# Kernel tuning notes

Measured on AMD Instinct MI355X. Metric: run time of the kernel, lower is better.

## Reference

```python
import jax, jax.numpy as jnp
import numpy as np

B, T_ENC, T_DEC = 32, 300, 500
N_MEL, ENC_DIM, ATT_RNN, DEC_RNN, PRE = 80, 512, 1024, 1024, 256
ATT_DIM, LOC_F, LOC_K = 128, 32, 31
PAD = (LOC_K - 1) // 2
P_PRENET = 0.1


def _w(k, shape, fan_in):
    return jax.random.normal(k, shape, jnp.float32) / np.float32(np.sqrt(fan_in))


def setup_inputs() -> dict:
    key = jax.random.key(0)
    ks = jax.random.split(key, 20)
    lens = jax.random.randint(ks[2], (B,), T_ENC // 2, T_ENC + 1).at[0].set(T_ENC)
    return {
        "memory": jax.random.normal(ks[0], (B, T_ENC, ENC_DIM), jnp.float32),
        "decoder_inputs": jax.random.normal(ks[1], (B, N_MEL, T_DEC), jnp.float32),
        "memory_lengths": lens,
        "pre_W1": _w(ks[3], (PRE, N_MEL), N_MEL),
        "pre_W2": _w(ks[4], (PRE, PRE), PRE),
        "att_Wih": _w(ks[5], (4 * ATT_RNN, PRE + ENC_DIM), PRE + ENC_DIM),
        "att_Whh": _w(ks[6], (4 * ATT_RNN, ATT_RNN), ATT_RNN),
        "att_bih": jnp.zeros((4 * ATT_RNN,), jnp.float32),
        "att_bhh": jnp.zeros((4 * ATT_RNN,), jnp.float32),
        "q_W": _w(ks[7], (ATT_DIM, ATT_RNN), ATT_RNN),
        "m_W": _w(ks[8], (ATT_DIM, ENC_DIM), ENC_DIM),
        "v_w": _w(ks[9], (ATT_DIM,), ATT_DIM),
        "loc_conv_W": _w(ks[10], (LOC_F, 2, LOC_K), 2 * LOC_K),
        "loc_dense_W": _w(ks[11], (ATT_DIM, LOC_F), LOC_F),
        "dec_Wih": _w(ks[12], (4 * DEC_RNN, ATT_RNN + ENC_DIM), ATT_RNN + ENC_DIM),
        "dec_Whh": _w(ks[13], (4 * DEC_RNN, DEC_RNN), DEC_RNN),
        "dec_bih": jnp.zeros((4 * DEC_RNN,), jnp.float32),
        "dec_bhh": jnp.zeros((4 * DEC_RNN,), jnp.float32),
        "proj_W": _w(ks[14], (N_MEL, DEC_RNN + ENC_DIM), DEC_RNN + ENC_DIM),
        "proj_b": jnp.zeros((N_MEL,), jnp.float32),
        "gate_W": _w(ks[15], (DEC_RNN + ENC_DIM,), DEC_RNN + ENC_DIM),
        "gate_b": jnp.zeros((), jnp.float32),
    }


def _lstm(x, h, c, Wih, Whh, bih, bhh):
    # PyTorch LSTMCell gate order: i, f, g, o
    g = x @ Wih.T + bih + h @ Whh.T + bhh
    i, f, gg, o = jnp.split(g, 4, axis=-1)
    c = jax.nn.sigmoid(f) * c + jax.nn.sigmoid(i) * jnp.tanh(gg)
    h = jax.nn.sigmoid(o) * jnp.tanh(c)
    return h, c


def _prenet(x, W1, W2):
    # Original uses F.dropout(..., 0.1, training=True) always; deterministic masks here.
    k1, k2 = jax.random.split(jax.random.key(1))
    x = jax.nn.relu(x @ W1.T)
    x = x * jax.random.bernoulli(k1, 1.0 - P_PRENET, x.shape) / (1.0 - P_PRENET)
    x = jax.nn.relu(x @ W2.T)
    x = x * jax.random.bernoulli(k2, 1.0 - P_PRENET, x.shape) / (1.0 - P_PRENET)
    return x


def _forward(memory, decoder_inputs, memory_lengths, pre_W1, pre_W2, att_Wih, att_Whh,
             att_bih, att_bhh, q_W, m_W, v_w, loc_conv_W, loc_dense_W, dec_Wih, dec_Whh,
             dec_bih, dec_bhh, proj_W, proj_b, gate_W, gate_b):
    x = jnp.transpose(decoder_inputs, (2, 0, 1))          # [T_dec, B, n_mel]
    go = jnp.zeros((1,) + x.shape[1:], x.dtype)
    x = jnp.concatenate([go, x], axis=0)                  # [T_dec+1, B, n_mel]
    dec_ins = _prenet(x, pre_W1, pre_W2)[:-1]             # [T_dec, B, PRE]

    processed_memory = memory @ m_W.T                     # [B, T_enc, ATT_DIM]
    valid = jnp.arange(T_ENC)[None, :] < memory_lengths[:, None]  # [B, T_enc]
    Bn = memory.shape[0]
    zf = lambda d: jnp.zeros((Bn, d), memory.dtype)
    carry0 = (zf(ATT_RNN), zf(ATT_RNN), zf(DEC_RNN), zf(DEC_RNN),
              zf(T_ENC), zf(T_ENC), zf(ENC_DIM))

    def step(carry, x_t):
        ah, ac, dh, dc, aw, awc, ctx = carry
        ah, ac = _lstm(jnp.concatenate([x_t, ctx], 1), ah, ac,
                       att_Wih, att_Whh, att_bih, att_bhh)
        awcat = jnp.stack([aw, awc], axis=1)              # [B, 2, T_enc]
        loc = jax.lax.conv_general_dilated(awcat, loc_conv_W, (1,), [(PAD, PAD)],
                                           dimension_numbers=('NCH', 'OIH', 'NCH'))
        loc = jnp.transpose(loc, (0, 2, 1)) @ loc_dense_W.T   # [B, T_enc, ATT_DIM]
        pq = (ah @ q_W.T)[:, None, :]                     # [B, 1, ATT_DIM]
        e = jnp.tanh(pq + loc + processed_memory) @ v_w   # [B, T_enc]
        e = jnp.where(valid, e, -jnp.inf)
        aw = jax.nn.softmax(e, axis=1)
        ctx = jnp.einsum('bt,btd->bd', aw, memory)        # [B, ENC_DIM]
        awc = awc + aw
        dh, dc = _lstm(jnp.concatenate([ah, ctx], 1), dh, dc,
                       dec_Wih, dec_Whh, dec_bih, dec_bhh)
        dhac = jnp.concatenate([dh, ctx], 1)
        mel = dhac @ proj_W.T + proj_b                    # [B, n_mel]
        gate = dhac @ gate_W + gate_b                     # [B]
        return (ah, ac, dh, dc, aw, awc, ctx), (mel, gate, aw)

    _, (mels, gates, aligns) = jax.lax.scan(jax.checkpoint(step), carry0, dec_ins)
    mel_outputs = jnp.transpose(mels, (1, 2, 0))          # [B, n_mel, T_dec]
    gate_outputs = gates.T                                # [B, T_dec]
    alignments = jnp.transpose(aligns, (1, 0, 2))         # [B, T_dec, T_enc]
    return mel_outputs, gate_outputs, alignments


def reference(memory, decoder_inputs, memory_lengths, pre_W1, pre_W2, att_Wih, att_Whh,
              att_bih, att_bhh, q_W, m_W, v_w, loc_conv_W, loc_dense_W, dec_Wih, dec_Whh,
              dec_bih, dec_bhh, proj_W, proj_b, gate_W, gate_b):
    return _forward(memory, decoder_inputs, memory_lengths, pre_W1, pre_W2, att_Wih,
                    att_Whh, att_bih, att_bhh, q_W, m_W, v_w, loc_conv_W, loc_dense_W,
                    dec_Wih, dec_Whh, dec_bih, dec_bhh, proj_W, proj_b, gate_W, gate_b)
```

## Files before the change

kernel.cpp:

```cpp
#include <hip/hip_runtime.h>

#define NB 32
#define TENC 300
#define TDEC 500
#define NMEL 80
#define ENCD 512
#define PRE 256
#define ADIM 128
#define RD 4
#define WSPLIT 2944

#define OFF_DECINS 0ull
#define OFF_WHI    2048000ull
#define OFF_AHR    4096000ull
#define OFF_DHR    (OFF_AHR + 131072ull)
#define OFF_CXR    (OFF_DHR + 131072ull)
#define RINGS_N    327680ull
#define OFF_WLO    (OFF_AHR + RINGS_N)
#define OFF_PM     8192000ull
#define OFF_STATE  (OFF_PM + 1228800ull)
#define OFF_AC     (OFF_STATE + 0ull)
#define OFF_DC     (OFF_STATE + 32768ull)
#define OFF_AW     (OFF_STATE + 65536ull)
#define OFF_AWC    (OFF_STATE + 75136ull)
#define OFF_E      (OFF_STATE + 84736ull)
#define OFF_SLOTS  (OFF_STATE + 94336ull)
#define STATE_N    98440ull
#define OFF_QWT    (OFF_STATE + STATE_N)
#define OFF_PROJWT (OFF_QWT + 131072ull)
#define OFF_MWT    (OFF_PROJWT + 122880ull)
#define OFF_W1T    (OFF_MWT + 65536ull)
#define OFF_W2T    (OFF_W1T + 20480ull)

__device__ __forceinline__ unsigned short f2bf(float f){
  unsigned u = __float_as_uint(f);
  unsigned r = (u + 0x7FFFu + ((u >> 16) & 1u)) >> 16;
  return (unsigned short)r;
}
__device__ __forceinline__ float bf2f(unsigned short h){
  return __uint_as_float(((unsigned)h) << 16);
}

__device__ __forceinline__ float gload(const float* p){
  return __hip_atomic_load(p, __ATOMIC_RELAXED, __HIP_MEMORY_SCOPE_AGENT);
}
__device__ __forceinline__ void gstore(float* p, float v){
  __hip_atomic_store(p, v, __ATOMIC_RELAXED, __HIP_MEMORY_SCOPE_AGENT);
}

__device__ __forceinline__ void gbar(unsigned* slots, unsigned epoch){
  __syncthreads();
  int tid = threadIdx.x;
  if (tid == 0)
    __hip_atomic_store(&slots[blockIdx.x], epoch, __ATOMIC_RELAXED, __HIP_MEMORY_SCOPE_AGENT);
  if (tid < 64){
    const unsigned long long* p = (const unsigned long long*)slots;
    unsigned long long a, b;
    do {
      a = __hip_atomic_load(p + 2*tid,     __ATOMIC_RELAXED, __HIP_MEMORY_SCOPE_AGENT);
      b = __hip_atomic_load(p + 2*tid + 1, __ATOMIC_RELAXED, __HIP_MEMORY_SCOPE_AGENT);
    } while ((unsigned)a < epoch || (unsigned)(a >> 32) < epoch ||
             (unsigned)b < epoch || (unsigned)(b >> 32) < epoch);
  }
  __syncthreads();
}

__host__ __device__ __forceinline__ unsigned rotl32(unsigned v, int r){ return (v<<r)|(v>>(32-r)); }

__host__ __device__ __forceinline__ void tf2x32(unsigned k0, unsigned k1, unsigned c0, unsigned c1,
                                                unsigned& y0, unsigned& y1){
  unsigned ks2 = k0 ^ k1 ^ 0x1BD11BDAu;
  unsigned x0 = c0 + k0, x1 = c1 + k1;
#define TFR(r) x0 += x1; x1 = rotl32(x1, r); x1 ^= x0;
  TFR(13) TFR(15) TFR(26) TFR(6)
  x0 += k1;  x1 += ks2 + 1u;
  TFR(17) TFR(29) TFR(16) TFR(24)
  x0 += ks2; x1 += k0 + 2u;
  TFR(13) TFR(15) TFR(26) TFR(6)
  x0 += k0;  x1 += k1 + 3u;
  TFR(17) TFR(29) TFR(16) TFR(24)
  x0 += k1;  x1 += ks2 + 4u;
  TFR(13) TFR(15) TFR(26) TFR(6)
  x0 += ks2; x1 += k0 + 5u;
#undef TFR
  y0 = x0; y1 = x1;
}

__device__ __forceinline__ float mask_scale(unsigned k0, unsigned k1, unsigned idx){
  unsigned y0, y1;
  tf2x32(k0, k1, 0u, idx, y0, y1);
  unsigned bits = y0 ^ y1;
  float u = __uint_as_float((bits >> 9) | 0x3f800000u) - 1.0f;
  return (u < 0.9f) ? (1.0f/0.9f) : 0.0f;
}

__global__ __launch_bounds__(256) void k_setup(float* __restrict__ ws,
    const float* __restrict__ qW, const float* __restrict__ projW, const float* __restrict__ mW,
    const float* __restrict__ w1, const float* __restrict__ w2,
    const float* __restrict__ dWih, const float* __restrict__ dWhh){
  long i = (long)blockIdx.x*256 + threadIdx.x;
  long stride = (long)gridDim.x*256;
  float* st = ws + OFF_STATE;
  for (long x = i; x < (long)STATE_N; x += stride) st[x] = 0.f;
  float* qWT = ws + OFF_QWT;
  for (long x = i; x < 1024*128; x += stride){ int u = x>>7, d = x&127; qWT[x] = qW[(size_t)d*1024+u]; }
  float* pWT = ws + OFF_PROJWT;
  for (long x = i; x < 1536*80; x += stride){ int k = x/80, m = x%80; pWT[x] = projW[(size_t)m*1536+k]; }
  float* mWT = ws + OFF_MWT;
  for (long x = i; x < 512*128; x += stride){ int k = x>>7, d = x&127; mWT[x] = mW[(size_t)d*512+k]; }
  float* w1T = ws + OFF_W1T;
  for (long x = i; x < 80*256; x += stride){ int m = x>>8, u = x&255; w1T[x] = w1[(size_t)u*80+m]; }
  float* w2T = ws + OFF_W2T;
  for (long x = i; x < 256*256; x += stride){ int k = x>>8, u = x&255; w2T[x] = w2[(size_t)u*256+k]; }
  unsigned short* wlo = (unsigned short*)(ws + OFF_WLO);
  for (long x = i; x < (long)WSPLIT*2560; x += stride){
    int row = (int)(x/2560), c = (int)(x%2560);
    float v = (c < 1536) ? dWih[(size_t)row*1536 + c] : dWhh[(size_t)row*1024 + (c-1536)];
    wlo[x] = f2bf(v);
  }
  unsigned short* whi = (unsigned short*)(ws + OFF_WHI);
  for (long x = i; x < (long)(4096-WSPLIT)*2560; x += stride){
    int row = WSPLIT + (int)(x/2560), c = (int)(x%2560);
    float v = (c < 1536) ? dWih[(size_t)row*1536 + c] : dWhh[(size_t)row*1024 + (c-1536)];
    whi[x] = f2bf(v);
  }
}

__global__ __launch_bounds__(256) void k_prenet(const float* __restrict__ di,
    const float* __restrict__ W1T, const float* __restrict__ W2T,
    unsigned short* __restrict__ dec_ins,
    unsigned k10, unsigned k11, unsigned k20, unsigned k21){
  __shared__ float xs[NMEL];
  __shared__ float h1s[PRE];
  int bid = blockIdx.x;
  int t = bid >> 5, b = bid & 31;
  int tid = threadIdx.x;
  if (tid < NMEL) xs[tid] = (t == 0) ? 0.f : di[(size_t)b*40000 + (size_t)tid*500 + (t-1)];
  __syncthreads();
  float acc = 0.f;
  for (int m = 0; m < NMEL; ++m) acc += xs[m] * W1T[m*256 + tid];
  acc = fmaxf(acc, 0.f);
  unsigned idx = (unsigned)bid*256u + (unsigned)tid;
  h1s[tid] = acc * mask_scale(k10, k11, idx);
  __syncthreads();
  float a2 = 0.f;
  for (int k = 0; k < PRE; ++k) a2 += h1s[k] * W2T[k*256 + tid];
  a2 = fmaxf(a2, 0.f);
  a2 *= mask_scale(k20, k21, idx);
  dec_ins[(size_t)bid*256 + tid] = f2bf(a2);
}

__global__ __launch_bounds__(128) void k_procmem(const float* __restrict__ mem,
    const float* __restrict__ mWT, float* __restrict__ pm){
  __shared__ float ms[ENCD];
  int bid = blockIdx.x;
  int tid = threadIdx.x;
  const float* src = mem + (size_t)bid*ENCD;
  for (int i = tid; i < ENCD; i += 128) ms[i] = src[i];
  __syncthreads();
  float acc = 0.f;
  for (int k = 0; k < ENCD; ++k) acc += ms[k] * mWT[k*128 + tid];
  pm[(size_t)bid*128 + tid] = acc;
}

template<bool S0B>
__device__ __forceinline__ float2 xld2(const void* s0v, int l0, const float* s1,
                                       const float* h, int b, int k){
  if (k < l0){
    if constexpr (S0B){
      const unsigned short* s0 = (const unsigned short*)s0v;
      unsigned u = *(const unsigned*)(s0 + (size_t)b*l0 + k);
      float2 r; r.x = __uint_as_float((u & 0xFFFFu) << 16); r.y = __uint_as_float((u >> 16) << 16);
      return r;
    } else {
      const float* s0 = (const float*)s0v;
      return *(const float2*)(s0 + (size_t)b*l0 + k);
    }
  }
  if (k < l0 + 512) return *(const float2*)(s1 + (b<<9) + (k - l0));
  return *(const float2*)(h + (b<<10) + (k - (l0 + 512)));
}

template<bool S0B, bool WB>
__device__ __forceinline__ void lstm_block(int ub,
    const float* __restrict__ W1, const float* __restrict__ W2,
    const unsigned short* __restrict__ wlo, const unsigned short* __restrict__ whi,
    const float* __restrict__ bih, const float* __restrict__ bhh,
    const void* __restrict__ s0, int l0, const float* __restrict__ s1,
    const float* __restrict__ hprev, int Ktot,
    float* __restrict__ c_st, float* __restrict__ hnew, int tid){
  __shared__ float Xc[2][128*32];
  __shared__ float gates[16][32];
  const int xw = l0 + 512, xw4 = xw >> 2;
  const int NC = Ktot >> 7;
  const int w = tid >> 6, l = tid & 63;
  const int ss = l & 31, ph = l >> 5;
  const int rlA = 2*w, rlB = 2*w + 1;
  const int rowA = (rlA >> 2)*1024 + ub*4 + (rlA & 3);
  const int rowB = (rlB >> 2)*1024 + ub*4 + (rlB & 3);
  const float4* W1A = (const float4*)(W1 + (size_t)rowA*xw);
  const float4* W1B = (const float4*)(W1 + (size_t)rowB*xw);
  const float4* W2A = (const float4*)(W2 + ((size_t)rowA<<10));
  const float4* W2B = (const float4*)(W2 + ((size_t)rowB<<10));
  const unsigned short* BA = nullptr; const unsigned short* BB = nullptr;
  if constexpr (WB){
    BA = (rowA < WSPLIT) ? wlo + (size_t)rowA*2560 : whi + (size_t)(rowA - WSPLIT)*2560;
    BB = (rowB < WSPLIT) ? wlo + (size_t)rowB*2560 : whi + (size_t)(rowB - WSPLIT)*2560;
  }
  auto loadWA = [&](int f)->float4{
    if constexpr (WB){
      ushort4 h4 = *(const ushort4*)(BA + 4*(size_t)f);
      return make_float4(bf2f(h4.x), bf2f(h4.y), bf2f(h4.z), bf2f(h4.w));
    } else return (f < xw4) ? W1A[f] : W2A[f - xw4];
  };
  auto loadWB = [&](int f)->float4{
    if constexpr (WB){
      ushort4 h4 = *(const ushort4*)(BB + 4*(size_t)f);
      return make_float4(bf2f(h4.x), bf2f(h4.y), bf2f(h4.z), bf2f(h4.w));
    } else return (f < xw4) ? W1B[f] : W2B[f - xw4];
  };
  float accA[16] = {}, accB[16] = {};
  float2 sx[4];
#pragma unroll
  for (int it = 0; it < 4; ++it){
    int pidx = tid + it*512;
    int b = pidx >> 6, kL = (pidx & 63)*2;
    sx[it] = xld2<S0B>(s0, l0, s1, hprev, b, kL);
  }
#pragma unroll
  for (int it = 0; it < 4; ++it){
    int pidx = tid + it*512;
    int b = pidx >> 6, kL = (pidx & 63)*2;
    int a0 = kL*32 + (((b>>2) ^ ((kL>>2)&7))<<2) + (b&3);
    Xc[0][a0] = sx[it].x; Xc[0][a0+32] = sx[it].y;
  }
  float4 wA = loadWA(ss), wB = loadWB(ss);
  __syncthreads();

  for (int c = 0; c < NC; ++c){
    float4 wAn, wBn;
    if (c + 1 < NC){
      int f = (c+1)*32 + ss;
      wAn = loadWA(f); wBn = loadWB(f);
      int kg0 = (c+1) << 7;
#pragma unroll
      for (int it = 0; it < 4; ++it){
        int pidx = tid + it*512;
        int b = pidx >> 6, kL = (pidx & 63)*2;
        sx[it] = xld2<S0B>(s0, l0, s1, hprev, b, kg0 + kL);
      }
    }
    const float4* X4 = (const float4*)Xc[c & 1];
    const int sw = ss & 7;
#pragma unroll
    for (int e = 0; e < 4; ++e){
      int kL = 4*ss + e;
      float ea = (e==0)?wA.x:(e==1)?wA.y:(e==2)?wA.z:wA.w;
      float eb = (e==0)?wB.x:(e==1)?wB.y:(e==2)?wB.z:wB.w;
      int base = kL*8;
#pragma unroll
      for (int j = 0; j < 4; ++j){
        int g = ph*4 + j;
        float4 xv = X4[base + (g ^ sw)];
        accA[4*j+0] += ea*xv.x; accA[4*j+1] += ea*xv.y;
        accA[4*j+2] += ea*xv.z; accA[4*j+3] += ea*xv.w;
        accB[4*j+0] += eb*xv.x; accB[4*j+1] += eb*xv.y;
        accB[4*j+2] += eb*xv.z; accB[4*j+3] += eb*xv.w;
      }
    }
    if (c + 1 < NC){
#pragma unroll
      for (int it = 0; it < 4; ++it){
        int pidx = tid + it*512;
        int b = pidx >> 6, kL = (pidx & 63)*2;
        int a0 = kL*32 + (((b>>2) ^ ((kL>>2)&7))<<2) + (b&3);
        Xc[(c+1)&1][a0] = sx[it].x; Xc[(c+1)&1][a0+32] = sx[it].y;
      }
      wA = wAn; wB = wBn;
    }
    __syncthreads();
  }
#pragma unroll
  for (int j = 0; j < 16; ++j){
    accA[j] += __shfl_xor(accA[j], 16, 64);
    accB[j] += __shfl_xor(accB[j], 16, 64);
  }
#pragma unroll
  for (int m = 8; m >= 1; m >>= 1){
    int up = ss & m;
#pragma unroll
    for (int j = 0; j < m; ++j){
      float sA = up ? accA[j] : accA[j+m];
      float kA = up ? accA[j+m] : accA[j];
      float sB = up ? accB[j] : accB[j+m];
      float kB = up ? accB[j+m] : accB[j];
      accA[j] = kA + __shfl_xor(sA, m, 64);
      accB[j] = kB + __shfl_xor(sB, m, 64);
    }
  }
  if (!(l & 16)){
    int b = ph*16 + (l & 15);
    gates[rlA][b] = accA[0];
    gates[rlB][b] = accB[0];
  }
  __syncthreads();
  if (tid < 128){
    int b = tid & 31, u = tid >> 5;
    int gu = ub*4 + u;
    float gi = gates[u][b]     + bih[gu]         + bhh[gu];
    float gf = gates[4+u][b]   + bih[1024+gu]    + bhh[1024+gu];
    float gg = gates[8+u][b]   + bih[2048+gu]    + bhh[2048+gu];
    float go = gates[12+u][b]  + bih[3072+gu]    + bhh[3072+gu];
    float ii = 1.f/(1.f + expf(-gi));
    float ff = 1.f/(1.f + expf(-gf));
    float oo = 1.f/(1.f + expf(-go));
    float tg = tanhf(gg);
    float cold = gload(&c_st[b*1024 + gu]);
    float cn = ff*cold + ii*tg;
    gstore(&c_st[b*1024 + gu], cn);
    gstore(&hnew[b*1024 + gu], oo*tanhf(cn));
  }
  __syncthreads();
}

__device__ __forceinline__ void energy_tile(int b, int tile, bool act, int h,
    const float* __restrict__ aw, const float* __restrict__ awc,
    const float* __restrict__ lcW, const float* __restrict__ ldW, const float* __restrict__ vw,
    const float* __restrict__ sPq, const float* __restrict__ pm, float* __restrict__ e_ws, int t2){
  __shared__ float sIn[2][2][46];
  __shared__ float cfs[2][16][33];
  __shared__ float ep[2][16][17];
  int j0 = tile*16;
  if (act){
    if (t2 < 46){ int j = j0 - 15 + t2; sIn[h][0][t2] = (j >= 0 && j < 300) ? gload(&aw[b*300 + j]) : 0.f; }
    else if (t2 < 92){ int i = t2 - 46; int j = j0 - 15 + i; sIn[h][1][i] = (j >= 0 && j < 300) ? gload(&awc[b*300 + j]) : 0.f; }
  }
  __syncthreads();
  if (act){
    int fg = t2 & 15, jl = t2 >> 4;
    int f0 = 2*fg;
    float c0 = 0.f, c1 = 0.f;
#pragma unroll
    for (int c = 0; c < 2; ++c)
#pragma unroll
      for (int k = 0; k < 31; ++k){
        float a = sIn[h][c][jl + k];
        c0 += a * lcW[f0*62 + c*31 + k];
        c1 += a * lcW[(f0+1)*62 + c*31 + k];
      }
    cfs[h][jl][f0] = c0; cfs[h][jl][f0+1] = c1;
  }
  __syncthreads();
  if (act){
    int dg = t2 & 15, jl = t2 >> 4;
    int j = j0 + jl;
    float s = 0.f;
    if (j < 300){
      const float* pmrow = pm + ((size_t)(b*300 + j))*128 + dg*8;
#pragma unroll
      for (int dd = 0; dd < 8; ++dd){
        int d = dg*8 + dd;
        float acc = sPq[d] + pmrow[dd];
#pragma unroll
        for (int f = 0; f < 32; ++f) acc += cfs[h][jl][f] * ldW[d*32 + f];
        s += vw[d] * tanhf(acc);
      }
    }
    ep[h][jl][dg] = s;
  }
  __syncthreads();
  if (act && t2 < 16){
    int j = j0 + t2;
    if (j < 300){
      float s = 0.f;
#pragma unroll
      for (int dg = 0; dg < 16; ++dg) s += ep[h][t2][dg];
      gstore(&e_ws[b*300 + j], s);
    }
  }
  __syncthreads();
}

__device__ __forceinline__ void pq_energy(int b, int jt, const float* __restrict__ ah,
    const float* __restrict__ qWT, const float* __restrict__ aw, const float* __restrict__ awc,
    const float* __restrict__ lcW, const float* __restrict__ ldW, const float* __restrict__ vw,
    const float* __restrict__ pm, float* __restrict__ e_ws, int tid){
  __shared__ float sAh[1024];
  __shared__ float pqs[512];
  __shared__ float sPq[128];
  for (int i = tid; i < 1024; i += 512) sAh[i] = ah[b*1024 + i];
  __syncthreads();
  int d = tid & 127, seg = tid >> 7;
  const float* qt = qWT + (size_t)(seg*256)*128 + d;
  const float* sh = sAh + seg*256;
  float a0 = 0.f, a1 = 0.f, a2 = 0.f, a3 = 0.f;
  for (int u = 0; u < 256; u += 4){
    a0 += sh[u]   * qt[(size_t)u*128];
    a1 += sh[u+1] * qt[(size_t)(u+1)*128];
    a2 += sh[u+2] * qt[(size_t)(u+2)*128];
    a3 += sh[u+3] * qt[(size_t)(u+3)*128];
  }
  pqs[seg*128 + d] = (a0 + a1) + (a2 + a3);
  __syncthreads();
  if (tid < 128) sPq[tid] = (pqs[tid] + pqs[128+tid]) + (pqs[256+tid] + pqs[384+tid]);
  __syncthreads();
  int h = tid >> 8, t2 = tid & 255;
  for (int r = 0; r < 2; ++r){
    int tile = r*16 + jt*2 + h;
    energy_tile(b, tile, tile < 19, h, aw, awc, lcW, ldW, vw, sPq, pm, e_ws, t2);
  }
}

__device__ __forceinline__ void dec_out_slice(int b, int jt,
    const float* __restrict__ dh, const float* __restrict__ ctx,
    const float* __restrict__ pWT, const float* __restrict__ projb,
    const float* __restrict__ gateW, const float* __restrict__ gateb,
    float* __restrict__ out, int s, int tid){
  __shared__ float sX[1536];
  __shared__ float melp[48][11];
  __shared__ float gatep[32];
  for (int i = tid; i < 1024; i += 512) sX[i] = dh[b*1024 + i];
  if (tid < 512) { int i = tid; sX[1024 + i] = ctx[b*512 + i]; }
  __syncthreads();
  if (tid < 480){
    int mi = tid % 10, kseg = tid / 10;
    int m = jt*10 + mi;
    const float* pw = pWT + m;
    int k0 = kseg*32;
    float a0 = 0.f, a1 = 0.f;
#pragma unroll 8
    for (int k = 0; k < 32; k += 2){
      a0 += sX[k0+k]   * pw[(size_t)(k0+k)*80];
      a1 += sX[k0+k+1] * pw[(size_t)(k0+k+1)*80];
    }
    melp[kseg][mi] = a0 + a1;
  } else if (jt == 0){
    int kseg = tid - 480;
    int k0 = kseg*48;
    float a = 0.f;
    for (int k = 0; k < 48; ++k) a += sX[k0+k] * gateW[k0+k];
    gatep[kseg] = a;
  }
  __syncthreads();
  if (tid < 10){
    float s2 = projb[jt*10 + tid];
    for (int q = 0; q < 48; ++q) s2 += melp[q][tid];
    out[(size_t)b*40000 + (size_t)(jt*10 + tid)*500 + s] = s2;
  }
  if (jt == 0 && tid == 10){
    float s2 = gateb[0];
    for (int q = 0; q < 32; ++q) s2 += gatep[q];
    out[1280000 + (size_t)b*500 + s] = s2;
  }
  __syncthreads();
}

__device__ __forceinline__ void soft_phase(int b, int dsl, const float* __restrict__ e_ws,
    const int* __restrict__ lens, const float* __restrict__ mem,
    float* __restrict__ aw, float* __restrict__ awc, float* __restrict__ ctx,
    float* __restrict__ out, int t, int tid){
  __shared__ float se[300];
  __shared__ float sa[300];
  __shared__ float red[512];
  int len = lens[b];
  for (int j = tid; j < 300; j += 512) se[j] = gload(&e_ws[b*300 + j]);
  __syncthreads();
  float m = -1e30f;
  for (int j = tid; j < len; j += 512) m = fmaxf(m, se[j]);
  red[tid] = m; __syncthreads();
  for (int s = 256; s > 0; s >>= 1){ if (tid < s) red[tid] = fmaxf(red[tid], red[tid + s]); __syncthreads(); }
  float mx = red[0]; __syncthreads();
  float ssum = 0.f;
  for (int j = tid; j < len; j += 512) ssum += expf(se[j] - mx);
  red[tid] = ssum; __syncthreads();
  for (int s = 256; s > 0; s >>= 1){ if (tid < s) red[tid] += red[tid + s]; __syncthreads(); }
  float inv = 1.f/red[0];
  __syncthreads();
  float* al = out + 1296000 + (size_t)b*150000 + (size_t)t*300;
  for (int j = tid; j < 300; j += 512){
    float v = (j < len) ? expf(se[j] - mx)*inv : 0.f;
    sa[j] = v;
    if (dsl == 0){
      gstore(&aw[b*300 + j], v);
      gstore(&awc[b*300 + j], gload(&awc[b*300 + j]) + v);
      al[j] = v;
    }
  }
  __syncthreads();
  int d = dsl*64 + (tid & 63), jq = tid >> 6;
  int chunk = (len + 7) >> 3;
  int j0 = jq*chunk, j1 = min(len, j0 + chunk);
  float a0 = 0.f, a1 = 0.f;
  const float* mb = mem + (size_t)b*153600 + d;
  int j = j0;
  for (; j + 1 < j1; j += 2){
    a0 += sa[j]   * mb[(size_t)j*512];
    a1 += sa[j+1] * mb[(size_t)(j+1)*512];
  }
  if (j < j1) a0 += sa[j]*mb[(size_t)j*512];
  red[tid] = a0 + a1; __syncthreads();
  if (jq == 0){
    int ln = tid & 63;
    float s = 0.f;
#pragma unroll
    for (int q = 0; q < 8; ++q) s += red[ln + 64*q];
    gstore(&ctx[b*512 + d], s);
  }
  __syncthreads();
}

struct DecParams {
  const float *memory;
  const int   *lens;
  const float *attWih, *attWhh, *attBih, *attBhh;
  const float *decBih, *decBhh;
  const float *lcW, *ldW, *vw, *projb, *gateW, *gateb;
  float *ws, *out;
};

__global__ void __launch_bounds__(512, 2) k_loop(DecParams p){
  int wg = blockIdx.x, tid = threadIdx.x;
  float* ws = p.ws;
  const unsigned short* decins = (const unsigned short*)(ws + OFF_DECINS);
  const unsigned short* wlo = (const unsigned short*)(ws + OFF_WLO);
  const unsigned short* whi = (const unsigned short*)(ws + OFF_WHI);
  float* e_ws = ws + OFF_E;
  float* pm = ws + OFF_PM;
  float* AC = ws + OFF_AC;
  float* DC = ws + OFF_DC;
  float* aw = ws + OFF_AW;
  float* awc = ws + OFF_AWC;
  float* qWT = ws + OFF_QWT;
  float* pWT = ws + OFF_PROJWT;
  unsigned* slots = (unsigned*)(ws + OFF_SLOTS);
  unsigned ep = 0;
  int b = wg >> 3, jt = wg & 7;

#define AHR(s) (ws + OFF_AHR + (size_t)(s)*32768)
#define DHR(s) (ws + OFF_DHR + (size_t)(s)*32768)
#define CXR(s) (ws + OFF_CXR + (size_t)(s)*16384)

  for (unsigned i = (unsigned)wg*512u + tid; i < (unsigned)RINGS_N; i += 131072u)
    gstore(ws + OFF_AHR + i, 0.f);
  gbar(slots, ++ep);

  lstm_block<true,false>(wg, p.attWih, p.attWhh, nullptr, nullptr, p.attBih, p.attBhh,
                         decins, PRE, CXR(0), AHR(0), 1792, AC, AHR(1), tid);
  gbar(slots, ++ep);

  for (int t = 0; t < TDEC; ++t){
    int cu = (t + 1) % RD, pr = t % RD, nx = (t + 2) % RD;
    pq_energy(b, jt, AHR(cu), qWT, aw, awc, p.lcW, p.ldW, p.vw, pm, e_ws, tid);
    if (t > 0)
      dec_out_slice(b, jt, DHR(pr), CXR(pr), pWT, p.projb, p.gateW, p.gateb, p.out, t - 1, tid);
    gbar(slots, ++ep);
    soft_phase(b, jt, e_ws, p.lens, p.memory, aw, awc, CXR(cu), p.out, t, tid);
    gbar(slots, ++ep);
    lstm_block<false,true>(wg, nullptr, nullptr, wlo, whi, p.decBih, p.decBhh,
                           AHR(cu), 1024, CXR(cu), DHR(pr), 2560, DC, DHR(cu), tid);
    if (t + 1 < TDEC)
      lstm_block<true,false>(wg, p.attWih, p.attWhh, nullptr, nullptr, p.attBih, p.attBhh,
                             decins + (size_t)(t + 1)*NB*PRE, PRE, CXR(cu), AHR(cu), 1792,
                             AC, AHR(nx), tid);
    gbar(slots, ++ep);
  }
  dec_out_slice(b, jt, DHR(500 % RD), CXR(500 % RD), pWT, p.projb, p.gateW, p.gateb,
                p.out, TDEC - 1, tid);
#undef AHR
#undef DHR
#undef CXR
}

extern "C" void kernel_launch(void* const* d_in, const int* in_sizes, int n_in,
                              void* d_out, int out_size, void* d_ws, size_t ws_size,
                              hipStream_t stream) {
  const float* memory   = (const float*)d_in[0];
  const float* dec_in   = (const float*)d_in[1];
  const int*   lens     = (const int*)  d_in[2];
  const float* pre_W1   = (const float*)d_in[3];
  const float* pre_W2   = (const float*)d_in[4];
  const float* att_Wih  = (const float*)d_in[5];
  const float* att_Whh  = (const float*)d_in[6];
  const float* att_bih  = (const float*)d_in[7];
  const float* att_bhh  = (const float*)d_in[8];
  const float* q_W      = (const float*)d_in[9];
  const float* m_W      = (const float*)d_in[10];
  const float* v_w      = (const float*)d_in[11];
  const float* lc_W     = (const float*)d_in[12];
  const float* ld_W     = (const float*)d_in[13];
  const float* dec_Wih  = (const float*)d_in[14];
  const float* dec_Whh  = (const float*)d_in[15];
  const float* dec_bih  = (const float*)d_in[16];
  const float* dec_bhh  = (const float*)d_in[17];
  const float* proj_W   = (const float*)d_in[18];
  const float* proj_b   = (const float*)d_in[19];
  const float* gate_W   = (const float*)d_in[20];
  const float* gate_b   = (const float*)d_in[21];
  float* out = (float*)d_out;
  float* ws  = (float*)d_ws;

  unsigned k10, k11, k20, k21;
  tf2x32(0u, 1u, 0u, 0u, k10, k11);
  tf2x32(0u, 1u, 0u, 1u, k20, k21);

  k_setup<<<1024, 256, 0, stream>>>(ws, q_W, proj_W, m_W, pre_W1, pre_W2, dec_Wih, dec_Whh);
  k_prenet<<<TDEC*NB, 256, 0, stream>>>(dec_in, ws + OFF_W1T, ws + OFF_W2T,
                                        (unsigned short*)(ws + OFF_DECINS), k10, k11, k20, k21);
  k_procmem<<<NB*TENC, 128, 0, stream>>>(memory, ws + OFF_MWT, ws + OFF_PM);

  DecParams hp;
  hp.memory = memory; hp.lens = lens;
  hp.attWih = att_Wih; hp.attWhh = att_Whh; hp.attBih = att_bih; hp.attBhh = att_bhh;
  hp.decBih = dec_bih; hp.decBhh = dec_bhh;
  hp.lcW = lc_W; hp.ldW = ld_W; hp.vw = v_w; hp.projb = proj_b; hp.gateW = gate_W; hp.gateb = gate_b;
  hp.ws = ws; hp.out = out;
  k_loop<<<256, 512, 0, stream>>>(hp);
}
```

Measured before the change: 77.00 ms.

## Double persistent workgroups to 512 and union shared memory across phases

Raises the persistent decoder kernel from 256 to 512 workgroups, so each workgroup computes 2 LSTM hidden units instead of 4, one energy tile instead of two, half as many context dimensions and 5 mel outputs instead of 10. Shared buffers from the separate phases are combined into one union to cut LDS per workgroup, and launch bounds are raised to allow 4 workgroups per CU so all 512 can be resident together. The grid barrier now polls 512 slots. Each workgroup's per-step weight streaming and serial work drops, but barrier polling gets wider, and per-thread register use must fit the higher occupancy target.

```diff
diff --git a/kernel.cpp b/kernel.cpp
--- a/kernel.cpp
+++ b/kernel.cpp
@@ -8,6 +8,7 @@
 #define PRE 256
 #define ADIM 128
 #define RD 4
+#define NBLK 512
 #define WSPLIT 2944
 
 #define OFF_DECINS 0ull
@@ -32,6 +33,14 @@
 #define OFF_W1T    (OFF_MWT + 65536ull)
 #define OFF_W2T    (OFF_W1T + 20480ull)
 
+union SMem {
+  struct { float Xc[2][4096]; float gates[8][32]; } lstm;
+  struct { float sAh[1024]; float pqs[512]; float sPq[128];
+           float sIn[2][2][46]; float cfs[2][16][33]; float ep[2][16][17]; } pq;
+  struct { float se[300]; float sa[300]; float red[512]; } soft;
+  struct { float sX[1536]; float melp[48][6]; float gatep[32]; } dout;
+};
+
 __device__ __forceinline__ unsigned short f2bf(float f){
   unsigned u = __float_as_uint(f);
   unsigned r = (u + 0x7FFFu + ((u >> 16) & 1u)) >> 16;
@@ -55,12 +64,16 @@
     __hip_atomic_store(&slots[blockIdx.x], epoch, __ATOMIC_RELAXED, __HIP_MEMORY_SCOPE_AGENT);
   if (tid < 64){
     const unsigned long long* p = (const unsigned long long*)slots;
-    unsigned long long a, b;
+    unsigned long long a, b, c, d;
     do {
-      a = __hip_atomic_load(p + 2*tid,     __ATOMIC_RELAXED, __HIP_MEMORY_SCOPE_AGENT);
-      b = __hip_atomic_load(p + 2*tid + 1, __ATOMIC_RELAXED, __HIP_MEMORY_SCOPE_AGENT);
+      a = __hip_atomic_load(p + 4*tid,     __ATOMIC_RELAXED, __HIP_MEMORY_SCOPE_AGENT);
+      b = __hip_atomic_load(p + 4*tid + 1, __ATOMIC_RELAXED, __HIP_MEMORY_SCOPE_AGENT);
+      c = __hip_atomic_load(p + 4*tid + 2, __ATOMIC_RELAXED, __HIP_MEMORY_SCOPE_AGENT);
+      d = __hip_atomic_load(p + 4*tid + 3, __ATOMIC_RELAXED, __HIP_MEMORY_SCOPE_AGENT);
     } while ((unsigned)a < epoch || (unsigned)(a >> 32) < epoch ||
-             (unsigned)b < epoch || (unsigned)(b >> 32) < epoch);
+             (unsigned)b < epoch || (unsigned)(b >> 32) < epoch ||
+             (unsigned)c < epoch || (unsigned)(c >> 32) < epoch ||
+             (unsigned)d < epoch || (unsigned)(d >> 32) < epoch);
   }
   __syncthreads();
 }
@@ -182,44 +195,30 @@
 }
 
 template<bool S0B, bool WB>
-__device__ __forceinline__ void lstm_block(int ub,
+__device__ __forceinline__ void lstm_block(SMem& sm, int ub,
     const float* __restrict__ W1, const float* __restrict__ W2,
     const unsigned short* __restrict__ wlo, const unsigned short* __restrict__ whi,
     const float* __restrict__ bih, const float* __restrict__ bhh,
     const void* __restrict__ s0, int l0, const float* __restrict__ s1,
     const float* __restrict__ hprev, int Ktot,
     float* __restrict__ c_st, float* __restrict__ hnew, int tid){
-  __shared__ float Xc[2][128*32];
-  __shared__ float gates[16][32];
   const int xw = l0 + 512, xw4 = xw >> 2;
   const int NC = Ktot >> 7;
   const int w = tid >> 6, l = tid & 63;
   const int ss = l & 31, ph = l >> 5;
-  const int rlA = 2*w, rlB = 2*w + 1;
-  const int rowA = (rlA >> 2)*1024 + ub*4 + (rlA & 3);
-  const int rowB = (rlB >> 2)*1024 + ub*4 + (rlB & 3);
-  const float4* W1A = (const float4*)(W1 + (size_t)rowA*xw);
-  const float4* W1B = (const float4*)(W1 + (size_t)rowB*xw);
-  const float4* W2A = (const float4*)(W2 + ((size_t)rowA<<10));
-  const float4* W2B = (const float4*)(W2 + ((size_t)rowB<<10));
-  const unsigned short* BA = nullptr; const unsigned short* BB = nullptr;
-  if constexpr (WB){
-    BA = (rowA < WSPLIT) ? wlo + (size_t)rowA*2560 : whi + (size_t)(rowA - WSPLIT)*2560;
-    BB = (rowB < WSPLIT) ? wlo + (size_t)rowB*2560 : whi + (size_t)(rowB - WSPLIT)*2560;
-  }
-  auto loadWA = [&](int f)->float4{
+  const int row = (w >> 1)*1024 + ub*2 + (w & 1);
+  const float4* W1A = (const float4*)(W1 + (size_t)row*xw);
+  const float4* W2A = (const float4*)(W2 + ((size_t)row<<10));
+  const unsigned short* BA = nullptr;
+  if constexpr (WB)
+    BA = (row < WSPLIT) ? wlo + (size_t)row*2560 : whi + (size_t)(row - WSPLIT)*2560;
+  auto loadW = [&](int f)->float4{
     if constexpr (WB){
       ushort4 h4 = *(const ushort4*)(BA + 4*(size_t)f);
       return make_float4(bf2f(h4.x), bf2f(h4.y), bf2f(h4.z), bf2f(h4.w));
     } else return (f < xw4) ? W1A[f] : W2A[f - xw4];
   };
-  auto loadWB = [&](int f)->float4{
-    if constexpr (WB){
-      ushort4 h4 = *(const ushort4*)(BB + 4*(size_t)f);
-      return make_float4(bf2f(h4.x), bf2f(h4.y), bf2f(h4.z), bf2f(h4.w));
-    } else return (f < xw4) ? W1B[f] : W2B[f - xw4];
-  };
-  float accA[16] = {}, accB[16] = {};
+  float acc[16] = {};
   float2 sx[4];
 #pragma unroll
   for (int it = 0; it < 4; ++it){
@@ -232,16 +231,15 @@
     int pidx = tid + it*512;
     int b = pidx >> 6, kL = (pidx & 63)*2;
     int a0 = kL*32 + (((b>>2) ^ ((kL>>2)&7))<<2) + (b&3);
-    Xc[0][a0] = sx[it].x; Xc[0][a0+32] = sx[it].y;
-  }
-  float4 wA = loadWA(ss), wB = loadWB(ss);
+    sm.lstm.Xc[0][a0] = sx[it].x; sm.lstm.Xc[0][a0+32] = sx[it].y;
+  }
+  float4 wA = loadW(ss);
   __syncthreads();
 
   for (int c = 0; c < NC; ++c){
-    float4 wAn, wBn;
+    float4 wAn;
     if (c + 1 < NC){
-      int f = (c+1)*32 + ss;
-      wAn = loadWA(f); wBn = loadWB(f);
+      wAn = loadW((c+1)*32 + ss);
       int kg0 = (c+1) << 7;
 #pragma unroll
       for (int it = 0; it < 4; ++it){
@@ -250,22 +248,18 @@
         sx[it] = xld2<S0B>(s0, l0, s1, hprev, b, kg0 + kL);
       }
     }
-    const float4* X4 = (const float4*)Xc[c & 1];
+    const float4* X4 = (const float4*)sm.lstm.Xc[c & 1];
     const int sw = ss & 7;
 #pragma unroll
     for (int e = 0; e < 4; ++e){
-      int kL = 4*ss + e;
       float ea = (e==0)?wA.x:(e==1)?wA.y:(e==2)?wA.z:wA.w;
-      float eb = (e==0)?wB.x:(e==1)?wB.y:(e==2)?wB.z:wB.w;
-      int base = kL*8;
+      int base = (4*ss + e)*8;
 #pragma unroll
       for (int j = 0; j < 4; ++j){
         int g = ph*4 + j;
         float4 xv = X4[base + (g ^ sw)];
-        accA[4*j+0] += ea*xv.x; accA[4*j+1] += ea*xv.y;
-        accA[4*j+2] += ea*xv.z; accA[4*j+3] += ea*xv.w;
-        accB[4*j+0] += eb*xv.x; accB[4*j+1] += eb*xv.y;
-        accB[4*j+2] += eb*xv.z; accB[4*j+3] += eb*xv.w;
+        acc[4*j+0] += ea*xv.x; acc[4*j+1] += ea*xv.y;
+        acc[4*j+2] += ea*xv.z; acc[4*j+3] += ea*xv.w;
       }
     }
     if (c + 1 < NC){
@@ -274,43 +268,35 @@
         int pidx = tid + it*512;
         int b = pidx >> 6, kL = (pidx & 63)*2;
         int a0 = kL*32 + (((b>>2) ^ ((kL>>2)&7))<<2) + (b&3);
-        Xc[(c+1)&1][a0] = sx[it].x; Xc[(c+1)&1][a0+32] = sx[it].y;
+        sm.lstm.Xc[(c+1)&1][a0] = sx[it].x; sm.lstm.Xc[(c+1)&1][a0+32] = sx[it].y;
       }
-      wA = wAn; wB = wBn;
+      wA = wAn;
     }
     __syncthreads();
   }
 #pragma unroll
-  for (int j = 0; j < 16; ++j){
-    accA[j] += __shfl_xor(accA[j], 16, 64);
-    accB[j] += __shfl_xor(accB[j], 16, 64);
-  }
+  for (int j = 0; j < 16; ++j)
+    acc[j] += __shfl_xor(acc[j], 16, 64);
 #pragma unroll
   for (int m = 8; m >= 1; m >>= 1){
     int up = ss & m;
 #pragma unroll
     for (int j = 0; j < m; ++j){
-      float sA = up ? accA[j] : accA[j+m];
-      float kA = up ? accA[j+m] : accA[j];
-      float sB = up ? accB[j] : accB[j+m];
-      float kB = up ? accB[j+m] : accB[j];
-      accA[j] = kA + __shfl_xor(sA, m, 64);
-      accB[j] = kB + __shfl_xor(sB, m, 64);
-    }
-  }
-  if (!(l & 16)){
-    int b = ph*16 + (l & 15);
-    gates[rlA][b] = accA[0];
-    gates[rlB][b] = accB[0];
-  }
-  __syncthreads();
-  if (tid < 128){
+      float sv = up ? acc[j] : acc[j+m];
+      float kv = up ? acc[j+m] : acc[j];
+      acc[j] = kv + __shfl_xor(sv, m, 64);
+    }
+  }
+  if (!(l & 16))
+    sm.lstm.gates[w][ph*16 + (l & 15)] = acc[0];
+  __syncthreads();
+  if (tid < 64){
     int b = tid & 31, u = tid >> 5;
-    int gu = ub*4 + u;
-    float gi = gates[u][b]     + bih[gu]         + bhh[gu];
-    float gf = gates[4+u][b]   + bih[1024+gu]    + bhh[1024+gu];
-    float gg = gates[8+u][b]   + bih[2048+gu]    + bhh[2048+gu];
-    float go = gates[12+u][b]  + bih[3072+gu]    + bhh[3072+gu];
+    int gu = ub*2 + u;
+    float gi = sm.lstm.gates[0+u][b] + bih[gu]         + bhh[gu];
+    float gf = sm.lstm.gates[2+u][b] + bih[1024+gu]    + bhh[1024+gu];
+    float gg = sm.lstm.gates[4+u][b] + bih[2048+gu]    + bhh[2048+gu];
+    float go = sm.lstm.gates[6+u][b] + bih[3072+gu]    + bhh[3072+gu];
     float ii = 1.f/(1.f + expf(-gi));
     float ff = 1.f/(1.f + expf(-gf));
     float oo = 1.f/(1.f + expf(-go));
@@ -323,17 +309,14 @@
   __syncthreads();
 }
 
-__device__ __forceinline__ void energy_tile(int b, int tile, bool act, int h,
+__device__ __forceinline__ void energy_tile(SMem& sm, int b, int tile, bool act, int h,
     const float* __restrict__ aw, const float* __restrict__ awc,
     const float* __restrict__ lcW, const float* __restrict__ ldW, const float* __restrict__ vw,
     const float* __restrict__ sPq, const float* __restrict__ pm, float* __restrict__ e_ws, int t2){
-  __shared__ float sIn[2][2][46];
-  __shared__ float cfs[2][16][33];
-  __shared__ float ep[2][16][17];
   int j0 = tile*16;
   if (act){
-    if (t2 < 46){ int j = j0 - 15 + t2; sIn[h][0][t2] = (j >= 0 && j < 300) ? gload(&aw[b*300 + j]) : 0.f; }
-    else if (t2 < 92){ int i = t2 - 46; int j = j0 - 15 + i; sIn[h][1][i] = (j >= 0 && j < 300) ? gload(&awc[b*300 + j]) : 0.f; }
+    if (t2 < 46){ int j = j0 - 15 + t2; sm.pq.sIn[h][0][t2] = (j >= 0 && j < 300) ? gload(&aw[b*300 + j]) : 0.f; }
+    else if (t2 < 92){ int i = t2 - 46; int j = j0 - 15 + i; sm.pq.sIn[h][1][i] = (j >= 0 && j < 300) ? gload(&awc[b*300 + j]) : 0.f; }
   }
   __syncthreads();
   if (act){
@@ -344,11 +327,11 @@
     for (int c = 0; c < 2; ++c)
 #pragma unroll
       for (int k = 0; k < 31; ++k){
-        float a = sIn[h][c][jl + k];
+        float a = sm.pq.sIn[h][c][jl + k];
         c0 += a * lcW[f0*62 + c*31 + k];
         c1 += a * lcW[(f0+1)*62 + c*31 + k];
       }
-    cfs[h][jl][f0] = c0; cfs[h][jl][f0+1] = c1;
+    sm.pq.cfs[h][jl][f0] = c0; sm.pq.cfs[h][jl][f0+1] = c1;
   }
   __syncthreads();
   if (act){
@@ -362,11 +345,11 @@
         int d = dg*8 + dd;
         float acc = sPq[d] + pmrow[dd];
 #pragma unroll
-        for (int f = 0; f < 32; ++f) acc += cfs[h][jl][f] * ldW[d*32 + f];
+        for (int f = 0; f < 32; ++f) acc += sm.pq.cfs[h][jl][f] * ldW[d*32 + f];
         s += vw[d] * tanhf(acc);
       }
     }
-    ep[h][jl][dg] = s;
+    sm.pq.ep[h][jl][dg] = s;
   }
   __syncthreads();
   if (act && t2 < 16){
@@ -374,25 +357,22 @@
     if (j < 300){
       float s = 0.f;
 #pragma unroll
-      for (int dg = 0; dg < 16; ++dg) s += ep[h][t2][dg];
+      for (int dg = 0; dg < 16; ++dg) s += sm.pq.ep[h][t2][dg];
       gstore(&e_ws[b*300 + j], s);
     }
   }
   __syncthreads();
 }
 
-__device__ __forceinline__ void pq_energy(int b, int jt, const float* __restrict__ ah,
+__device__ __forceinline__ void pq_energy(SMem& sm, int b, int sl, const float* __restrict__ ah,
     const float* __restrict__ qWT, const float* __restrict__ aw, const float* __restrict__ awc,
     const float* __restrict__ lcW, const float* __restrict__ ldW, const float* __restrict__ vw,
     const float* __restrict__ pm, float* __restrict__ e_ws, int tid){
-  __shared__ float sAh[1024];
-  __shared__ float pqs[512];
-  __shared__ float sPq[128];
-  for (int i = tid; i < 1024; i += 512) sAh[i] = ah[b*1024 + i];
+  for (int i = tid; i < 1024; i += 512) sm.pq.sAh[i] = ah[b*1024 + i];
   __syncthreads();
   int d = tid & 127, seg = tid >> 7;
   const float* qt = qWT + (size_t)(seg*256)*128 + d;
-  const float* sh = sAh + seg*256;
+  const float* sh = sm.pq.sAh + seg*256;
   float a0 = 0.f, a1 = 0.f, a2 = 0.f, a3 = 0.f;
   for (int u = 0; u < 256; u += 4){
     a0 += sh[u]   * qt[(size_t)u*128];
@@ -400,110 +380,102 @@
     a2 += sh[u+2] * qt[(size_t)(u+2)*128];
     a3 += sh[u+3] * qt[(size_t)(u+3)*128];
   }
-  pqs[seg*128 + d] = (a0 + a1) + (a2 + a3);
-  __syncthreads();
-  if (tid < 128) sPq[tid] = (pqs[tid] + pqs[128+tid]) + (pqs[256+tid] + pqs[384+tid]);
+  sm.pq.pqs[seg*128 + d] = (a0 + a1) + (a2 + a3);
+  __syncthreads();
+  if (tid < 128) sm.pq.sPq[tid] = (sm.pq.pqs[tid] + sm.pq.pqs[128+tid]) + (sm.pq.pqs[256+tid] + sm.pq.pqs[384+tid]);
   __syncthreads();
   int h = tid >> 8, t2 = tid & 255;
-  for (int r = 0; r < 2; ++r){
-    int tile = r*16 + jt*2 + h;
-    energy_tile(b, tile, tile < 19, h, aw, awc, lcW, ldW, vw, sPq, pm, e_ws, t2);
-  }
-}
-
-__device__ __forceinline__ void dec_out_slice(int b, int jt,
+  int tile = sl*2 + h;
+  energy_tile(sm, b, tile, tile < 19, h, aw, awc, lcW, ldW, vw, sm.pq.sPq, pm, e_ws, t2);
+}
+
+__device__ __forceinline__ void dec_out_slice(SMem& sm, int b, int sl,
     const float* __restrict__ dh, const float* __restrict__ ctx,
     const float* __restrict__ pWT, const float* __restrict__ projb,
     const float* __restrict__ gateW, const float* __restrict__ gateb,
     float* __restrict__ out, int s, int tid){
-  __shared__ float sX[1536];
-  __shared__ float melp[48][11];
-  __shared__ float gatep[32];
-  for (int i = tid; i < 1024; i += 512) sX[i] = dh[b*1024 + i];
-  if (tid < 512) { int i = tid; sX[1024 + i] = ctx[b*512 + i]; }
-  __syncthreads();
-  if (tid < 480){
-    int mi = tid % 10, kseg = tid / 10;
-    int m = jt*10 + mi;
+  for (int i = tid; i < 1024; i += 512) sm.dout.sX[i] = dh[b*1024 + i];
+  if (tid < 512) sm.dout.sX[1024 + tid] = ctx[b*512 + tid];
+  __syncthreads();
+  if (tid < 240){
+    int mi = tid % 5, kseg = tid / 5;
+    int m = sl*5 + mi;
     const float* pw = pWT + m;
     int k0 = kseg*32;
     float a0 = 0.f, a1 = 0.f;
 #pragma unroll 8
     for (int k = 0; k < 32; k += 2){
-      a0 += sX[k0+k]   * pw[(size_t)(k0+k)*80];
-      a1 += sX[k0+k+1] * pw[(size_t)(k0+k+1)*80];
-    }
-    melp[kseg][mi] = a0 + a1;
-  } else if (jt == 0){
-    int kseg = tid - 480;
+      a0 += sm.dout.sX[k0+k]   * pw[(size_t)(k0+k)*80];
+      a1 += sm.dout.sX[k0+k+1] * pw[(size_t)(k0+k+1)*80];
+    }
+    sm.dout.melp[kseg][mi] = a0 + a1;
+  } else if (sl == 0 && tid < 272){
+    int kseg = tid - 240;
     int k0 = kseg*48;
     float a = 0.f;
-    for (int k = 0; k < 48; ++k) a += sX[k0+k] * gateW[k0+k];
-    gatep[kseg] = a;
-  }
-  __syncthreads();
-  if (tid < 10){
-    float s2 = projb[jt*10 + tid];
-    for (int q = 0; q < 48; ++q) s2 += melp[q][tid];
-    out[(size_t)b*40000 + (size_t)(jt*10 + tid)*500 + s] = s2;
-  }
-  if (jt == 0 && tid == 10){
+    for (int k = 0; k < 48; ++k) a += sm.dout.sX[k0+k] * gateW[k0+k];
+    sm.dout.gatep[kseg] = a;
+  }
+  __syncthreads();
+  if (tid < 5){
+    float s2 = projb[sl*5 + tid];
+    for (int q = 0; q < 48; ++q) s2 += sm.dout.melp[q][tid];
+    out[(size_t)b*40000 + (size_t)(sl*5 + tid)*500 + s] = s2;
+  }
+  if (sl == 0 && tid == 5){
     float s2 = gateb[0];
-    for (int q = 0; q < 32; ++q) s2 += gatep[q];
+    for (int q = 0; q < 32; ++q) s2 += sm.dout.gatep[q];
     out[1280000 + (size_t)b*500 + s] = s2;
   }
   __syncthreads();
 }
 
-__device__ __forceinline__ void soft_phase(int b, int dsl, const float* __restrict__ e_ws,
+__device__ __forceinline__ void soft_phase(SMem& sm, int b, int sl, const float* __restrict__ e_ws,
     const int* __restrict__ lens, const float* __restrict__ mem,
     float* __restrict__ aw, float* __restrict__ awc, float* __restrict__ ctx,
     float* __restrict__ out, int t, int tid){
-  __shared__ float se[300];
-  __shared__ float sa[300];
-  __shared__ float red[512];
   int len = lens[b];
-  for (int j = tid; j < 300; j += 512) se[j] = gload(&e_ws[b*300 + j]);
+  for (int j = tid; j < 300; j += 512) sm.soft.se[j] = gload(&e_ws[b*300 + j]);
   __syncthreads();
   float m = -1e30f;
-  for (int j = tid; j < len; j += 512) m = fmaxf(m, se[j]);
-  red[tid] = m; __syncthreads();
-  for (int s = 256; s > 0; s >>= 1){ if (tid < s) red[tid] = fmaxf(red[tid], red[tid + s]); __syncthreads(); }
-  float mx = red[0]; __syncthreads();
+  for (int j = tid; j < len; j += 512) m = fmaxf(m, sm.soft.se[j]);
+  sm.soft.red[tid] = m; __syncthreads();
+  for (int s = 256; s > 0; s >>= 1){ if (tid < s) sm.soft.red[tid] = fmaxf(sm.soft.red[tid], sm.soft.red[tid + s]); __syncthreads(); }
+  float mx = sm.soft.red[0]; __syncthreads();
   float ssum = 0.f;
-  for (int j = tid; j < len; j += 512) ssum += expf(se[j] - mx);
-  red[tid] = ssum; __syncthreads();
-  for (int s = 256; s > 0; s >>= 1){ if (tid < s) red[tid] += red[tid + s]; __syncthreads(); }
-  float inv = 1.f/red[0];
+  for (int j = tid; j < len; j += 512) ssum += expf(sm.soft.se[j] - mx);
+  sm.soft.red[tid] = ssum; __syncthreads();
+  for (int s = 256; s > 0; s >>= 1){ if (tid < s) sm.soft.red[tid] += sm.soft.red[tid + s]; __syncthreads(); }
+  float inv = 1.f/sm.soft.red[0];
   __syncthreads();
   float* al = out + 1296000 + (size_t)b*150000 + (size_t)t*300;
   for (int j = tid; j < 300; j += 512){
-    float v = (j < len) ? expf(se[j] - mx)*inv : 0.f;
-    sa[j] = v;
-    if (dsl == 0){
+    float v = (j < len) ? expf(sm.soft.se[j] - mx)*inv : 0.f;
+    sm.soft.sa[j] = v;
+    if (sl == 0){
       gstore(&aw[b*300 + j], v);
       gstore(&awc[b*300 + j], gload(&awc[b*300 + j]) + v);
       al[j] = v;
     }
   }
   __syncthreads();
-  int d = dsl*64 + (tid & 63), jq = tid >> 6;
-  int chunk = (len + 7) >> 3;
+  int d = sl*32 + (tid & 31), jq = tid >> 5;
+  int chunk = (len + 15) >> 4;
   int j0 = jq*chunk, j1 = min(len, j0 + chunk);
   float a0 = 0.f, a1 = 0.f;
   const float* mb = mem + (size_t)b*153600 + d;
   int j = j0;
   for (; j + 1 < j1; j += 2){
-    a0 += sa[j]   * mb[(size_t)j*512];
-    a1 += sa[j+1] * mb[(size_t)(j+1)*512];
-  }
-  if (j < j1) a0 += sa[j]*mb[(size_t)j*512];
-  red[tid] = a0 + a1; __syncthreads();
+    a0 += sm.soft.sa[j]   * mb[(size_t)j*512];
+    a1 += sm.soft.sa[j+1] * mb[(size_t)(j+1)*512];
+  }
+  if (j < j1) a0 += sm.soft.sa[j]*mb[(size_t)j*512];
+  sm.soft.red[tid] = a0 + a1; __syncthreads();
   if (jq == 0){
-    int ln = tid & 63;
+    int ln = tid & 31;
     float s = 0.f;
 #pragma unroll
-    for (int q = 0; q < 8; ++q) s += red[ln + 64*q];
+    for (int q = 0; q < 16; ++q) s += sm.soft.red[ln + 32*q];
     gstore(&ctx[b*512 + d], s);
   }
   __syncthreads();
@@ -518,7 +490,8 @@
   float *ws, *out;
 };
 
-__global__ void __launch_bounds__(512, 2) k_loop(DecParams p){
+__global__ void __launch_bounds__(512, 4) k_loop(DecParams p){
+  __shared__ SMem sm;
   int wg = blockIdx.x, tid = threadIdx.x;
   float* ws = p.ws;
   const unsigned short* decins = (const unsigned short*)(ws + OFF_DECINS);
@@ -534,37 +507,37 @@
   float* pWT = ws + OFF_PROJWT;
   unsigned* slots = (unsigned*)(ws + OFF_SLOTS);
   unsigned ep = 0;
-  int b = wg >> 3, jt = wg & 7;
+  int b = wg >> 4, sl = wg & 15;
 
 #define AHR(s) (ws + OFF_AHR + (size_t)(s)*32768)
 #define DHR(s) (ws + OFF_DHR + (size_t)(s)*32768)
 #define CXR(s) (ws + OFF_CXR + (size_t)(s)*16384)
 
-  for (unsigned i = (unsigned)wg*512u + tid; i < (unsigned)RINGS_N; i += 131072u)
+  for (unsigned i = (unsigned)wg*512u + tid; i < (unsigned)RINGS_N; i += 262144u)
     gstore(ws + OFF_AHR + i, 0.f);
   gbar(slots, ++ep);
 
-  lstm_block<true,false>(wg, p.attWih, p.attWhh, nullptr, nullptr, p.attBih, p.attBhh,
+  lstm_block<true,false>(sm, wg, p.attWih, p.attWhh, nullptr, nullptr, p.attBih, p.attBhh,
                          decins, PRE, CXR(0), AHR(0), 1792, AC, AHR(1), tid);
   gbar(slots, ++ep);
 
   for (int t = 0; t < TDEC; ++t){
     int cu = (t + 1) % RD, pr = t % RD, nx = (t + 2) % RD;
-    pq_energy(b, jt, AHR(cu), qWT, aw, awc, p.lcW, p.ldW, p.vw, pm, e_ws, tid);
+    pq_energy(sm, b, sl, AHR(cu), qWT, aw, awc, p.lcW, p.ldW, p.vw, pm, e_ws, tid);
     if (t > 0)
-      dec_out_slice(b, jt, DHR(pr), CXR(pr), pWT, p.projb, p.gateW, p.gateb, p.out, t - 1, tid);
+      dec_out_slice(sm, b, sl, DHR(pr), CXR(pr), pWT, p.projb, p.gateW, p.gateb, p.out, t - 1, tid);
     gbar(slots, ++ep);
-    soft_phase(b, jt, e_ws, p.lens, p.memory, aw, awc, CXR(cu), p.out, t, tid);
+    soft_phase(sm, b, sl, e_ws, p.lens, p.memory, aw, awc, CXR(cu), p.out, t, tid);
     gbar(slots, ++ep);
-    lstm_block<false,true>(wg, nullptr, nullptr, wlo, whi, p.decBih, p.decBhh,
+    lstm_block<false,true>(sm, wg, nullptr, nullptr, wlo, whi, p.decBih, p.decBhh,
                            AHR(cu), 1024, CXR(cu), DHR(pr), 2560, DC, DHR(cu), tid);
     if (t + 1 < TDEC)
-      lstm_block<true,false>(wg, p.attWih, p.attWhh, nullptr, nullptr, p.attBih, p.attBhh,
+      lstm_block<true,false>(sm, wg, p.attWih, p.attWhh, nullptr, nullptr, p.attBih, p.attBhh,
                              decins + (size_t)(t + 1)*NB*PRE, PRE, CXR(cu), AHR(cu), 1792,
                              AC, AHR(nx), tid);
     gbar(slots, ++ep);
   }
-  dec_out_slice(b, jt, DHR(500 % RD), CXR(500 % RD), pWT, p.projb, p.gateW, p.gateb,
+  dec_out_slice(sm, b, sl, DHR(500 % RD), CXR(500 % RD), pWT, p.projb, p.gateW, p.gateb,
                 p.out, TDEC - 1, tid);
 #undef AHR
 #undef DHR
@@ -614,5 +587,5 @@
   hp.decBih = dec_bih; hp.decBhh = dec_bhh;
   hp.lcW = lc_W; hp.ldW = ld_W; hp.vw = v_w; hp.projb = proj_b; hp.gateW = gate_W; hp.gateb = gate_b;
   hp.ws = ws; hp.out = out;
-  k_loop<<<256, 512, 0, stream>>>(hp);
-}
+  k_loop<<<NBLK, 512, 0, stream>>>(hp);
+}
```

Result: slower. 101.5 ms (+31.8%).
